# Performance work log

Measured on AMD Instinct MI355X. Metric: run time of the kernel, lower is better.

The kernel has to match this reference:

```python
import jax, jax.numpy as jnp
import numpy as np

T, B, I, H, R, O = 128, 32, 128, 128, 100, 64


def setup_inputs() -> dict:
    key = jax.random.key(0)
    ks = jax.random.split(key, 8)
    # xavier-ish / kaiming-ish scales so tanh doesn't saturate
    return {
        "x": jax.random.normal(ks[0], (T, B, I), jnp.float32),
        "C": jax.random.uniform(ks[1], (R, R), jnp.float32) / R,
        "W_ih": jax.random.normal(ks[2], (R, I, H), jnp.float32) * (1.0 / np.sqrt(I)),
        "W_hh": jax.random.normal(ks[3], (R, H, H), jnp.float32) * (1.0 / np.sqrt(H)),
        "W_rhh": jax.random.normal(ks[4], (R, H, H), jnp.float32) * (1.0 / np.sqrt(H)),
        "bias": jax.random.normal(ks[5], (R, H), jnp.float32) * 0.1,
        "W_out": jax.random.normal(ks[6], (R * H, O), jnp.float32) * (1.0 / np.sqrt(R * H)),
        "b_out": jax.random.normal(ks[7], (O,), jnp.float32) * 0.1,
    }


def reference(x, C, W_ih, W_hh, W_rhh, bias, b_out, W_out):
    seq_len, bs, _ = x.shape
    num_regions, hidden = bias.shape
    H0 = jnp.zeros((num_regions, bs, hidden), dtype=x.dtype)

    def step(Hprev, x_t):
        # input drive: per-region projection of the shared input
        inp = jnp.einsum('bi,rih->rbh', x_t, W_ih)
        # local recurrence
        loc = jnp.einsum('rbh,rhg->rbg', Hprev, W_hh)
        # connectome-weighted message sum: recurrent_sum[j] = sum_i C[i,j] * Hprev[i]
        msg = jnp.einsum('ij,ibh->jbh', C, Hprev)
        cross = jnp.einsum('rbh,rhg->rbg', msg, W_rhh)
        Ht = jnp.tanh(inp + loc + cross + bias[:, None, :])
        return Ht, Ht

    _, H_hist = jax.lax.scan(step, H0, x)          # [T, R, B, H]
    H_hist = H_hist.transpose(0, 2, 1, 3).reshape(seq_len, bs, num_regions * hidden)
    return H_hist @ W_out + b_out                   # [T, B, O]
```

## Files before the change

### kernel.cpp

```cpp
#include <hip/hip_runtime.h>
#include <hip/hip_bf16.h>

typedef unsigned char u8;
typedef unsigned short u16;
typedef __attribute__((ext_vector_type(8))) short bf16x8;
typedef __attribute__((ext_vector_type(8))) _Float16 f16x8;
typedef __attribute__((ext_vector_type(4))) float f32x4;
typedef __attribute__((ext_vector_type(2))) float f32x2;
typedef __attribute__((ext_vector_type(4))) int i32x4;
typedef __attribute__((ext_vector_type(2))) int i32x2;

#define T_ 128
#define B_ 32
#define I_ 128
#define H_ 128
#define R_ 100
#define O_ 64
#define NWG2 200
#define NRED 4
#define SLICE (R_*B_*H_)
#define ROWB  (B_*H_)
#define XOFF  (T_*B_*I_)
#define WOFF  (R_*H_*H_)
#define OOFF  (O_*R_*H_)
#define PB    (16*O_)

__device__ __forceinline__ float b2f(u16 u) {
  unsigned x = ((unsigned)u) << 16; float f; __builtin_memcpy(&f, &x, 4); return f;
}
__device__ __forceinline__ u16 f2b(float f) {
  unsigned x; __builtin_memcpy(&x, &f, 4);
  unsigned lsb = (x >> 16) & 1u;
  x += 0x7fffu + lsb;
  return (u16)(x >> 16);
}
__device__ __forceinline__ void split2(float f, u16& hi, u16& lo) {
  hi = f2b(f);
  lo = f2b(f - b2f(hi));
}
__device__ __forceinline__ u16 f2h(float f) {
  _Float16 h = (_Float16)f; u16 u; __builtin_memcpy(&u, &h, 2); return u;
}
__device__ __forceinline__ float h2f(u16 u) {
  _Float16 h; __builtin_memcpy(&h, &u, 2); return (float)h;
}
__device__ __forceinline__ void split2h(float f, u16& hi, u16& lo) {
  _Float16 h = (_Float16)f;
  _Float16 l = (_Float16)(f - (float)h);
  __builtin_memcpy(&hi, &h, 2); __builtin_memcpy(&lo, &l, 2);
}
__device__ __forceinline__ float fast_tanh(float v) {
  float a = fabsf(v);
  float e = __expf(-2.f * a);
  float th = (1.f - e) * __builtin_amdgcn_rcpf(1.f + e);
  return v < 0.f ? -th : th;
}

#if __has_builtin(__builtin_amdgcn_cvt_pk_f32_fp8) && __has_builtin(__builtin_amdgcn_cvt_pk_fp8_f32)
#define HW_FP8 1
#endif

__device__ __forceinline__ unsigned enc1_fp8(float f) {
  unsigned x; __builtin_memcpy(&x, &f, 4);
  unsigned s = (x >> 31) << 7;
  float a = fabsf(f);
  if (!(a < 464.f)) return s | 0x7E;
  if (a == 0.f) return s;
  int E = (int)((x >> 23) & 0xFF) - 127;
  if (E < -6) E = -6;
  float sc; unsigned sb = (unsigned)(127 + 3 - E) << 23; __builtin_memcpy(&sc, &sb, 4);
  int q = (int)rintf(a * sc);
  if (q == 16) { E += 1; q = 8; }
  if (E > 8) return s | 0x7E;
  unsigned ee, mm;
  if (q < 8) { ee = 0; mm = (unsigned)q; }
  else { ee = (unsigned)(E + 7); mm = (unsigned)(q - 8); }
  return s | (ee << 3) | mm;
}
__device__ __forceinline__ float dec1_fp8(unsigned b) {
  unsigned s = (b >> 7) & 1, ee = (b >> 3) & 0xF, mm = b & 7;
  float v;
  if (ee == 0) v = (float)mm * 0.001953125f;
  else { unsigned fb = ((ee + 120) << 23) | (mm << 20); __builtin_memcpy(&v, &fb, 4); }
  return s ? -v : v;
}
__device__ __forceinline__ void fp8x4_to_f32(unsigned u, float* o) {
#ifdef HW_FP8
  f32x2 a = __builtin_amdgcn_cvt_pk_f32_fp8((int)u, false);
  f32x2 b = __builtin_amdgcn_cvt_pk_f32_fp8((int)u, true);
  o[0] = a[0]; o[1] = a[1]; o[2] = b[0]; o[3] = b[1];
#else
  o[0] = dec1_fp8(u & 255); o[1] = dec1_fp8((u >> 8) & 255);
  o[2] = dec1_fp8((u >> 16) & 255); o[3] = dec1_fp8(u >> 24);
#endif
}
__device__ __forceinline__ unsigned f32x4_to_fp8(float f0, float f1, float f2, float f3) {
#ifdef HW_FP8
  int v = __builtin_amdgcn_cvt_pk_fp8_f32(f0, f1, 0, false);
  v = __builtin_amdgcn_cvt_pk_fp8_f32(f2, f3, v, true);
  return (unsigned)v;
#else
  return enc1_fp8(f0) | (enc1_fp8(f1) << 8) | (enc1_fp8(f2) << 16) | (enc1_fp8(f3) << 24);
#endif
}
__device__ __forceinline__ i32x4 pack16(const u16* p) {
  i32x4 o;
  #pragma unroll
  for (int g = 0; g < 4; ++g)
    o[g] = (int)f32x4_to_fp8(h2f(p[g*4+0]), h2f(p[g*4+1]), h2f(p[g*4+2]), h2f(p[g*4+3]));
  return o;
}

__device__ __forceinline__ void st16_sc(void* p, i32x4 v) {
  asm volatile("global_store_dwordx4 %0, %1, off sc1" :: "v"(p), "v"(v) : "memory");
}
__device__ __forceinline__ void ld4_issue(int& r, const void* p) {
  asm volatile("global_load_dword %0, %1, off sc1" : "=v"(r) : "v"(p));
}
__device__ __forceinline__ void wait_vm() { asm volatile("s_waitcnt vmcnt(0)" ::: "memory"); }
#define WAITV(N) do { asm volatile("s_waitcnt vmcnt(" #N ")" ::: "memory"); \
                      __builtin_amdgcn_sched_barrier(0); } while (0)

__device__ __forceinline__ float aldf(const float* p) {
  return __hip_atomic_load((float*)p, __ATOMIC_RELAXED, __HIP_MEMORY_SCOPE_AGENT);
}
__device__ __forceinline__ void astf(float* p, float v) {
  __hip_atomic_store(p, v, __ATOMIC_RELAXED, __HIP_MEMORY_SCOPE_AGENT);
}

__global__ void __launch_bounds__(256)
probe_dtype(const u16* __restrict__ x, int* __restrict__ mode)
{
  __shared__ int cnt;
  if (threadIdx.x == 0) cnt = 0;
  __syncthreads();
  int bad = 0;
  for (int i = threadIdx.x; i < 8192; i += 256) {
    int ex = (x[i] >> 7) & 0xFF;
    if (ex >= 134) ++bad;
  }
  atomicAdd(&cnt, bad);
  __syncthreads();
  if (threadIdx.x == 0) *mode = (cnt > 256) ? 1 : 0;
}

__device__ __forceinline__ float load_in(const void* p, size_t i, int f32) {
  return f32 ? ((const float*)p)[i] : b2f(((const u16*)p)[i]);
}

__global__ void __launch_bounds__(256)
conv_split(const void* __restrict__ src, u16* __restrict__ hi, u16* __restrict__ lo,
           const int* __restrict__ mode, int n)
{
  int i = blockIdx.x * 256 + threadIdx.x;
  if (i < n) { u16 h, l; split2(load_in(src, i, *mode), h, l); hi[i] = h; lo[i] = l; }
}

__global__ void __launch_bounds__(256)
conv_vec(const void* __restrict__ src, float* __restrict__ dst,
         const int* __restrict__ mode, int n)
{
  int i = blockIdx.x * 256 + threadIdx.x;
  if (i < n) dst[i] = load_in(src, i, *mode);
}

__global__ void __launch_bounds__(256)
transpose_kn2(const void* __restrict__ in, u16* __restrict__ ohi, u16* __restrict__ olo,
              int KK, int NN, const int* __restrict__ mode, int fmt)
{
  __shared__ float tile[32][33];
  const int f32 = *mode;
  int ntk = KK >> 5, ntn = NN >> 5;
  int bid = blockIdx.x;
  int m  = bid / (ntk * ntn);
  int rem = bid % (ntk * ntn);
  int kt = rem / ntn, nt = rem % ntn;
  size_t base = (size_t)m * KK * NN;
  int tid = threadIdx.x;
  int tc = tid & 31, tr0 = tid >> 5;
  #pragma unroll
  for (int rr = 0; rr < 4; ++rr) {
    int tr = tr0 + rr * 8;
    tile[tr][tc] = load_in(in, base + (size_t)(kt*32 + tr) * NN + nt*32 + tc, f32);
  }
  __syncthreads();
  #pragma unroll
  for (int rr = 0; rr < 4; ++rr) {
    int tr = tr0 + rr * 8;
    u16 h, l;
    if (fmt) split2h(tile[tc][tr], h, l); else split2(tile[tc][tr], h, l);
    size_t di = base + (size_t)(nt*32 + tr) * KK + kt*32 + tc;
    ohi[di] = h; olo[di] = l;
  }
}

__device__ __forceinline__ void wait_flags(const int* f, int cnt, int target, int tid) {
  if (tid < cnt) {
    int sp = 0;
    while (__hip_atomic_load((int*)&f[tid * 32], __ATOMIC_RELAXED, __HIP_MEMORY_SCOPE_AGENT) < target) {
      __builtin_amdgcn_s_sleep(2);
      if (++sp > (1 << 18)) break;
    }
  }
  asm volatile("" ::: "memory");
  __syncthreads();
}
__device__ __forceinline__ void poll1(const int* f, int target) {
  int sp = 0;
  while (__hip_atomic_load((int*)f, __ATOMIC_RELAXED, __HIP_MEMORY_SCOPE_AGENT) < target) {
    if (++sp > 48) __builtin_amdgcn_s_sleep(2);
    if (sp > (1 << 20)) break;
  }
  asm volatile("" ::: "memory");
}
__device__ __forceinline__ void post_flag(int* f, int v) {
  __hip_atomic_store(f, v, __ATOMIC_RELAXED, __HIP_MEMORY_SCOPE_AGENT);
}

__device__ __forceinline__ f32x4 mfma_(bf16x8 a, bf16x8 b, f32x4 c) {
  return __builtin_amdgcn_mfma_f32_16x16x32_bf16(a, b, c, 0, 0, 0);
}
__device__ __forceinline__ f32x4 mfma_h(f16x8 a, f16x8 b, f32x4 c) {
  return __builtin_amdgcn_mfma_f32_16x16x32_f16(a, b, c, 0, 0, 0);
}

#define MIXROW(Q, CI) do { \
  float c_ = csh[(CI)]; float tf_[4]; \
  fp8x4_to_f32((unsigned)(Q), tf_); \
  macc0 = fmaf(c_, tf_[0], macc0); macc1 = fmaf(c_, tf_[1], macc1); \
  macc2 = fmaf(c_, tf_[2], macc2); macc3 = fmaf(c_, tf_[3], macc3); \
} while (0)

#define ISSUE8(Q, P) do { _Pragma("unroll") \
  for (int k_ = 0; k_ < 8; ++k_) ld4_issue(Q[k_], (P) + (size_t)k_ * ROWB); } while (0)
#define ISSUE4(Q, P) do { _Pragma("unroll") \
  for (int k_ = 0; k_ < 4; ++k_) ld4_issue(Q[k_], (P) + (size_t)k_ * ROWB); } while (0)
#define PROC8(Q, CI) do { _Pragma("unroll") \
  for (int k_ = 0; k_ < 8; ++k_) MIXROW(Q[k_], (CI) + k_); } while (0)
#define PROC4(Q, CI) do { _Pragma("unroll") \
  for (int k_ = 0; k_ < 4; ++k_) MIXROW(Q[k_], (CI) + k_); } while (0)

__global__ void __launch_bounds__(512)
rnn_kernel(const u16* __restrict__ x,
           u8* __restrict__ Hb,
           const u16* __restrict__ WihT, const u16* __restrict__ WhhT,
           const u16* __restrict__ WrhhT,
           const float* __restrict__ Cf,
           const float* __restrict__ biasf,
           const u16* __restrict__ WoutT,
           float* __restrict__ part,
           u16* __restrict__ part2,
           const float* __restrict__ boutf,
           float* __restrict__ out, int* __restrict__ flags, int bigpart)
{
  const int w    = blockIdx.x;
  const int tid  = threadIdx.x;
  const int lane = tid & 63;
  const int wv   = tid >> 6;
  const int l15  = lane & 15;
  const int quad = lane >> 4;

  __shared__ __align__(16) u16 Hmhi[16 * 136];
  __shared__ __align__(16) u16 Hmlo[16 * 136];
  __shared__ __align__(16) u16 msgS[16 * 136];
  __shared__ __align__(16) u16 mS[16 * 128];
  __shared__ float csh[112];

  if (w >= NWG2) {
    const int aw = w - NWG2;
    for (int t = 0; t < T_; ++t) {
      wait_flags(flags + 1, NWG2, t + 1, tid);
      const float* pb = part + (size_t)(t & 1) * (NWG2 * PB);
      int e = aw * 512 + tid;
      int b = e >> 6, o = e & 63;
      int ue = b >> 4, bl = b & 15;
      float s = 0.f;
      #pragma unroll 4
      for (int r2 = 0; r2 < R_; ++r2)
        s += aldf(pb + (size_t)(r2 * 2 + ue) * PB + bl * O_ + o);
      out[(size_t)t * (B_*O_) + e] = s + boutf[o];
    }
    return;
  }

  const int r = w >> 1;
  const int u = w & 1;
  const int col = wv * 16 + l15;

  for (int e = tid; e < 16 * 136; e += 512) { Hmhi[e] = 0; Hmlo[e] = 0; }
  if (tid < R_) csh[tid] = Cf[(size_t)tid * R_ + r];
  __syncthreads();

  for (int t = 0; t < T_; ++t) {
    f32x4 accX = {0,0,0,0}, accH = {0,0,0,0};
    {
      const u16* Ax  = x + (size_t)t * (B_*I_) + (size_t)(u*16) * I_;
      const u16* Bw0 = WihT + (size_t)r * (H_*I_);
      const u16* Bw1 = WhhT + (size_t)r * (H_*H_);
      #pragma unroll
      for (int kk = 0; kk < 4; ++kk) {
        int koff = kk * 32 + quad * 8;
        {
          const u16* pa = Ax + (size_t)l15 * 128 + koff;
          bf16x8 ah = *(const bf16x8*)pa, al = *(const bf16x8*)(pa + XOFF);
          const u16* pb = Bw0 + (size_t)col * 128 + koff;
          bf16x8 bh = *(const bf16x8*)pb, bl = *(const bf16x8*)(pb + WOFF);
          accX = mfma_(al,bh, mfma_(ah,bl, mfma_(ah,bh, accX)));
        }
        {
          bf16x8 ah = *(const bf16x8*)(&Hmhi[l15 * 136 + koff]);
          bf16x8 al = *(const bf16x8*)(&Hmlo[l15 * 136 + koff]);
          const u16* pb = Bw1 + (size_t)col * 128 + koff;
          bf16x8 bh = *(const bf16x8*)pb, bl = *(const bf16x8*)(pb + WOFF);
          accH = mfma_(al,bh, mfma_(ah,bl, mfma_(ah,bh, accH)));
        }
      }
    }

    if (t > 0) {
      if (tid < R_) poll1(&flags[(tid * 2 + u) * 32], t);
      __syncthreads();

      const u8* Hs = Hb + (size_t)((t + 1) & 1) * SLICE
                   + (size_t)(u*16 + (tid >> 5)) * H_ + (tid & 31) * 4;
      float macc0=0.f, macc1=0.f, macc2=0.f, macc3=0.f;
      int bufA[8], bufB[8], bufC[8];
      const u8* pI = Hs;
      ISSUE8(bufA, pI); pI += (size_t)8 * ROWB;
      ISSUE8(bufB, pI); pI += (size_t)8 * ROWB;
      ISSUE8(bufC, pI); pI += (size_t)8 * ROWB;
      int ci = 0;
      for (int it = 0; it < 3; ++it) {
        WAITV(16); PROC8(bufA, ci); ci += 8; ISSUE8(bufA, pI); pI += (size_t)8 * ROWB;
        WAITV(16); PROC8(bufB, ci); ci += 8; ISSUE8(bufB, pI); pI += (size_t)8 * ROWB;
        WAITV(16); PROC8(bufC, ci); ci += 8; ISSUE8(bufC, pI); pI += (size_t)8 * ROWB;
      }
      WAITV(16); PROC8(bufA, 72); ISSUE4(bufA, pI);
      WAITV(12); PROC8(bufB, 80);
      WAITV(4);  PROC8(bufC, 88);
      WAITV(0);  PROC4(bufA, 96);

      union { u16 h[4]; unsigned long long v; } mw;
      mw.h[0]=f2h(macc0); mw.h[1]=f2h(macc1); mw.h[2]=f2h(macc2); mw.h[3]=f2h(macc3);
      *(unsigned long long*)&msgS[(tid >> 5) * 136 + (tid & 31) * 4] = mw.v;
      __syncthreads();

      {
        const u16* Bw2 = WrhhT + (size_t)r * (H_*H_);
        #pragma unroll
        for (int kk = 0; kk < 4; ++kk) {
          int koff = kk * 32 + quad * 8;
          f16x8 a0 = *(const f16x8*)(&msgS[l15 * 136 + koff]);
          const u16* pb = Bw2 + (size_t)col * 128 + koff;
          f16x8 bh = *(const f16x8*)pb, bl = *(const f16x8*)(pb + WOFF);
          accX = mfma_h(a0, bl, mfma_h(a0, bh, accX));
        }
      }
    } else {
      __syncthreads();
    }

    {
      float bs = biasf[r*H_ + col];
      #pragma unroll
      for (int rr = 0; rr < 4; ++rr) {
        int br = quad*4 + rr;
        u16 h, l;
        float v = fast_tanh(accX[rr] + accH[rr] + bs);
        split2(v, h, l);
        Hmhi[br*136 + col] = h; Hmlo[br*136 + col] = l;
        mS[br*128 + col] = f2h(v);
      }
    }
    __syncthreads();

    if (tid < 64) {
      int row = tid >> 2, c = (tid & 3) * 32;
      u8* Hn = Hb + (size_t)(t & 1) * SLICE + (size_t)r * ROWB
             + (size_t)(u*16 + row) * H_ + c;
      const u16* p = &mS[row * 128 + c];
      st16_sc(Hn,      pack16(p));
      st16_sc(Hn + 16, pack16(p + 16));
      wait_vm();
      if (tid == 0) post_flag(&flags[w * 32 + 0], t + 1);
    }

    {
      if (wv >= 4) {
        const int o = (wv - 4) * 16 + l15;
        const u16* Bo = WoutT + (size_t)o * (R_*H_) + (size_t)r * H_;
        f32x4 y0 = {0,0,0,0};
        #pragma unroll
        for (int kk = 0; kk < 4; ++kk) {
          int koff = kk * 32 + quad * 8;
          bf16x8 ah = *(const bf16x8*)(&Hmhi[l15 * 136 + koff]);
          bf16x8 al = *(const bf16x8*)(&Hmlo[l15 * 136 + koff]);
          bf16x8 bh = *(const bf16x8*)(Bo + koff);
          bf16x8 bl = *(const bf16x8*)(Bo + OOFF + koff);
          y0 = mfma_(al,bh, mfma_(ah,bl, mfma_(ah,bh, y0)));
        }
        if (bigpart) {
          u16* pp = part2 + ((size_t)t * R_ + r) * (B_*O_);
          #pragma unroll
          for (int rr = 0; rr < 4; ++rr)
            pp[(u*16 + quad*4 + rr)*O_ + o] = f2b(y0[rr]);
        } else {
          float* pp = part + (size_t)(t & 1) * (NWG2 * PB) + (size_t)w * PB;
          #pragma unroll
          for (int rr = 0; rr < 4; ++rr)
            astf(pp + (quad*4 + rr)*O_ + o, y0[rr]);
        }
      }
      if (!bigpart) {
        __syncthreads();
        if (tid == 0) post_flag(&flags[w * 32 + 1], t + 1);
      }
    }
  }
}

__global__ void __launch_bounds__(256)
reduce_out(const u16* __restrict__ part2, const float* __restrict__ boutf,
           float* __restrict__ out)
{
  const int t = blockIdx.x, tid = threadIdx.x;
  const u16* base = part2 + (size_t)t * R_ * (B_*O_) + tid * 8;
  float acc[8] = {0,0,0,0,0,0,0,0};
  for (int r2 = 0; r2 < R_; ++r2) {
    bf16x8 v = *(const bf16x8*)(base + (size_t)r2 * (B_*O_));
    #pragma unroll
    for (int j = 0; j < 8; ++j) acc[j] += b2f((u16)v[j]);
  }
  int e = tid * 8;
  #pragma unroll
  for (int j = 0; j < 8; ++j)
    out[(size_t)t * (B_*O_) + e + j] = acc[j] + boutf[(e + j) & (O_-1)];
}

extern "C" void kernel_launch(void* const* d_in, const int* in_sizes, int n_in,
                              void* d_out, int out_size, void* d_ws, size_t ws_size,
                              hipStream_t stream) {
  const void* xp    = d_in[0];
  const void* Cp    = d_in[1];
  const void* Wih   = d_in[2];
  const void* Whh   = d_in[3];
  const void* Wrhh  = d_in[4];
  const void* biasp = d_in[5];
  const void* Wout  = d_in[6];
  const void* boutp = d_in[7];
  float* outp = (float*)d_out;

  char* ws = (char*)d_ws;
  size_t off = 0;
  auto carve = [&](size_t bytes) -> void* {
    void* p = ws + off;
    off += (bytes + 255) & ~(size_t)255;
    return p;
  };
  u16*   xb    = (u16*)carve((size_t)2 * XOFF * 2);
  u8*    Hb    = (u8*)carve((size_t)2 * SLICE);
  u16*   wihT  = (u16*)carve((size_t)2 * WOFF * 2);
  u16*   whhT  = (u16*)carve((size_t)2 * WOFF * 2);
  u16*   wrhhT = (u16*)carve((size_t)2 * WOFF * 2);
  u16*   woutT = (u16*)carve((size_t)2 * OOFF * 2);
  float* cfp   = (float*)carve((size_t)R_ * R_ * 4);
  float* biasf = (float*)carve((size_t)R_ * H_ * 4);
  float* boutf = (float*)carve((size_t)O_ * 4);
  float* partp = (float*)carve((size_t)2 * NWG2 * PB * 4);
  int*   flagp = (int*)carve((size_t)256 * 32 * 4);
  int*   modep = (int*)carve(256);
  size_t part2_bytes = (size_t)T_ * R_ * B_ * O_ * 2;
  u16*   part2 = (u16*)(ws + off);
  int bigpart = (off + part2_bytes) <= ws_size;

  hipMemsetAsync(flagp, 0, (size_t)256 * 32 * 4, stream);

  probe_dtype<<<dim3(1), dim3(256), 0, stream>>>((const u16*)xp, modep);
  conv_split<<<dim3((XOFF + 255)/256), dim3(256), 0, stream>>>(xp, xb, xb + XOFF, modep, XOFF);
  conv_vec<<<dim3((R_*H_ + 255)/256), dim3(256), 0, stream>>>(biasp, biasf, modep, R_*H_);
  conv_vec<<<dim3(1), dim3(256), 0, stream>>>(boutp, boutf, modep, O_);
  conv_vec<<<dim3((R_*R_ + 255)/256), dim3(256), 0, stream>>>(Cp, cfp, modep, R_*R_);

  transpose_kn2<<<dim3(R_ * 16), dim3(256), 0, stream>>>(Wih,  wihT,  wihT  + WOFF, I_, H_, modep, 0);
  transpose_kn2<<<dim3(R_ * 16), dim3(256), 0, stream>>>(Whh,  whhT,  whhT  + WOFF, H_, H_, modep, 0);
  transpose_kn2<<<dim3(R_ * 16), dim3(256), 0, stream>>>(Wrhh, wrhhT, wrhhT + WOFF, H_, H_, modep, 1);
  transpose_kn2<<<dim3(800),     dim3(256), 0, stream>>>(Wout, woutT, woutT + OOFF, R_ * H_, O_, modep, 0);

  int nblk = bigpart ? NWG2 : (NWG2 + NRED);
  rnn_kernel<<<dim3(nblk), dim3(512), 0, stream>>>(
      xb, Hb, wihT, whhT, wrhhT, cfp, biasf, woutT,
      partp, part2, boutf, outp, flagp, bigpart);

  if (bigpart)
    reduce_out<<<dim3(T_), dim3(256), 0, stream>>>(part2, boutf, outp);
}
```

Measured before the change: 1.218 ms.

## Stage per-step hidden state into per-XCD copies for local L2 reads

At each step, up to four workgroups on each XCD copy the previous hidden state from the shared buffer, which is read with sc1 loads, into a per-XCD staged buffer, then post per-chunk flags. All workgroups on that XCD then read the connectome mix inputs from the staged copy using sc0 loads, which should hit that XCD's L2 instead of going coherent across dies. The W_rhh tiles are also loaded before the mix wait so they overlap the polling. The cost is an extra copy and flag handshake on the critical path of every timestep, plus reliance on the hardware XCC id register and on co-residency assumptions.

```diff
diff --git a/kernel.cpp b/kernel.cpp
--- a/kernel.cpp
+++ b/kernel.cpp
@@ -24,6 +24,11 @@
 #define WOFF  (R_*H_*H_)
 #define OOFF  (O_*R_*H_)
 #define PB    (16*O_)
+#define UHALF 2048
+#define SBUF  (R_*UHALF)
+#define CHUNK (50*UHALF)
+#define SFBASE 6400
+#define XCNTOFF 7168
 
 __device__ __forceinline__ float b2f(u16 u) {
   unsigned x = ((unsigned)u) << 16; float f; __builtin_memcpy(&f, &x, 4); return f;
@@ -114,8 +119,11 @@
 __device__ __forceinline__ void st16_sc(void* p, i32x4 v) {
   asm volatile("global_store_dwordx4 %0, %1, off sc1" :: "v"(p), "v"(v) : "memory");
 }
-__device__ __forceinline__ void ld4_issue(int& r, const void* p) {
-  asm volatile("global_load_dword %0, %1, off sc1" : "=v"(r) : "v"(p));
+__device__ __forceinline__ void ld4_issue0(int& r, const void* p) {
+  asm volatile("global_load_dword %0, %1, off sc0" : "=v"(r) : "v"(p));
+}
+__device__ __forceinline__ void ld16_issue1(i32x4& r, const void* p) {
+  asm volatile("global_load_dwordx4 %0, %1, off sc1" : "=v"(r) : "v"(p));
 }
 __device__ __forceinline__ void wait_vm() { asm volatile("s_waitcnt vmcnt(0)" ::: "memory"); }
 #define WAITV(N) do { asm volatile("s_waitcnt vmcnt(" #N ")" ::: "memory"); \
@@ -232,9 +240,9 @@
 } while (0)
 
 #define ISSUE8(Q, P) do { _Pragma("unroll") \
-  for (int k_ = 0; k_ < 8; ++k_) ld4_issue(Q[k_], (P) + (size_t)k_ * ROWB); } while (0)
+  for (int k_ = 0; k_ < 8; ++k_) ld4_issue0(Q[k_], (P) + (size_t)k_ * UHALF); } while (0)
 #define ISSUE4(Q, P) do { _Pragma("unroll") \
-  for (int k_ = 0; k_ < 4; ++k_) ld4_issue(Q[k_], (P) + (size_t)k_ * ROWB); } while (0)
+  for (int k_ = 0; k_ < 4; ++k_) ld4_issue0(Q[k_], (P) + (size_t)k_ * UHALF); } while (0)
 #define PROC8(Q, CI) do { _Pragma("unroll") \
   for (int k_ = 0; k_ < 8; ++k_) MIXROW(Q[k_], (CI) + k_); } while (0)
 #define PROC4(Q, CI) do { _Pragma("unroll") \
@@ -243,6 +251,7 @@
 __global__ void __launch_bounds__(512)
 rnn_kernel(const u16* __restrict__ x,
            u8* __restrict__ Hb,
+           u8* __restrict__ staged,
            const u16* __restrict__ WihT, const u16* __restrict__ WhhT,
            const u16* __restrict__ WrhhT,
            const float* __restrict__ Cf,
@@ -265,6 +274,7 @@
   __shared__ __align__(16) u16 msgS[16 * 136];
   __shared__ __align__(16) u16 mS[16 * 128];
   __shared__ float csh[112];
+  __shared__ int shRank, shN;
 
   if (w >= NWG2) {
     const int aw = w - NWG2;
@@ -283,6 +293,13 @@
     return;
   }
 
+  int xcd;
+  asm volatile("s_getreg_b32 %0, hwreg(HW_REG_XCC_ID)" : "=s"(xcd));
+  xcd &= 7;
+  if (tid == 0)
+    shRank = __hip_atomic_fetch_add(&flags[XCNTOFF + xcd], 1,
+                                    __ATOMIC_RELAXED, __HIP_MEMORY_SCOPE_AGENT);
+
   const int r = w >> 1;
   const int u = w & 1;
   const int col = wv * 16 + l15;
@@ -290,6 +307,7 @@
   for (int e = tid; e < 16 * 136; e += 512) { Hmhi[e] = 0; Hmlo[e] = 0; }
   if (tid < R_) csh[tid] = Cf[(size_t)tid * R_ + r];
   __syncthreads();
+  const int rank = shRank;
 
   for (int t = 0; t < T_; ++t) {
     f32x4 accX = {0,0,0,0}, accH = {0,0,0,0};
@@ -318,22 +336,74 @@
     }
 
     if (t > 0) {
-      if (tid < R_) poll1(&flags[(tid * 2 + u) * 32], t);
+      if (t == 1) {
+        if (tid == 0) {
+          int c = __hip_atomic_load(&flags[XCNTOFF + xcd],
+                                    __ATOMIC_RELAXED, __HIP_MEMORY_SCOPE_AGENT);
+          shN = c < 1 ? 1 : (c > 4 ? 4 : c);
+        }
+        __syncthreads();
+      }
+      const int par = (t + 1) & 1;
+
+      f16x8 w2h[4], w2l[4];
+      {
+        const u16* Bw2 = WrhhT + (size_t)r * (H_*H_);
+        #pragma unroll
+        for (int kk = 0; kk < 4; ++kk) {
+          const u16* pb = Bw2 + (size_t)col * 128 + kk*32 + quad*8;
+          w2h[kk] = *(const f16x8*)pb;
+          w2l[kk] = *(const f16x8*)(pb + WOFF);
+        }
+      }
+
+      if (rank < 4) {
+        const int N = shN;
+        for (int cc = rank; cc < 4; cc += N) {
+          const int su = cc & 1, sc2 = cc >> 1;
+          if (tid < 50) poll1(&flags[(((sc2*50 + tid) << 1) | su) * 32], t);
+          __syncthreads();
+          const u8* srcb = Hb + (size_t)par * SLICE;
+          u8* dstb = staged + ((((size_t)xcd << 1) | par) * 2 + su) * SBUF
+                   + (size_t)sc2 * CHUNK;
+          i32x4 qq[13];
+          #pragma unroll
+          for (int k = 0; k < 13; ++k) {
+            int le = tid * 16 + k * 8192;
+            int le2 = le < CHUNK ? le : 0;
+            int reg = sc2 * 50 + (le2 >> 11);
+            ld16_issue1(qq[k], srcb + (size_t)reg * ROWB + su * UHALF + (le2 & 2047));
+          }
+          WAITV(0);
+          #pragma unroll
+          for (int k = 0; k < 13; ++k) {
+            int le = tid * 16 + k * 8192;
+            if (le < CHUNK) *(i32x4*)(dstb + le) = qq[k];
+          }
+          wait_vm();
+          __syncthreads();
+          if (tid == 0)
+            post_flag(&flags[SFBASE + ((xcd * 2 + par) << 2) + cc], t);
+        }
+      }
+
+      if (tid < 2)
+        poll1(&flags[SFBASE + ((xcd * 2 + par) << 2) + u + (tid << 1)], t);
       __syncthreads();
 
-      const u8* Hs = Hb + (size_t)((t + 1) & 1) * SLICE
-                   + (size_t)(u*16 + (tid >> 5)) * H_ + (tid & 31) * 4;
+      const u8* Ms = staged + ((((size_t)xcd << 1) | par) * 2 + u) * SBUF
+                   + (size_t)(tid >> 5) * 128 + (tid & 31) * 4;
       float macc0=0.f, macc1=0.f, macc2=0.f, macc3=0.f;
       int bufA[8], bufB[8], bufC[8];
-      const u8* pI = Hs;
-      ISSUE8(bufA, pI); pI += (size_t)8 * ROWB;
-      ISSUE8(bufB, pI); pI += (size_t)8 * ROWB;
-      ISSUE8(bufC, pI); pI += (size_t)8 * ROWB;
+      const u8* pI = Ms;
+      ISSUE8(bufA, pI); pI += (size_t)8 * UHALF;
+      ISSUE8(bufB, pI); pI += (size_t)8 * UHALF;
+      ISSUE8(bufC, pI); pI += (size_t)8 * UHALF;
       int ci = 0;
       for (int it = 0; it < 3; ++it) {
-        WAITV(16); PROC8(bufA, ci); ci += 8; ISSUE8(bufA, pI); pI += (size_t)8 * ROWB;
-        WAITV(16); PROC8(bufB, ci); ci += 8; ISSUE8(bufB, pI); pI += (size_t)8 * ROWB;
-        WAITV(16); PROC8(bufC, ci); ci += 8; ISSUE8(bufC, pI); pI += (size_t)8 * ROWB;
+        WAITV(16); PROC8(bufA, ci); ci += 8; ISSUE8(bufA, pI); pI += (size_t)8 * UHALF;
+        WAITV(16); PROC8(bufB, ci); ci += 8; ISSUE8(bufB, pI); pI += (size_t)8 * UHALF;
+        WAITV(16); PROC8(bufC, ci); ci += 8; ISSUE8(bufC, pI); pI += (size_t)8 * UHALF;
       }
       WAITV(16); PROC8(bufA, 72); ISSUE4(bufA, pI);
       WAITV(12); PROC8(bufB, 80);
@@ -345,16 +415,11 @@
       *(unsigned long long*)&msgS[(tid >> 5) * 136 + (tid & 31) * 4] = mw.v;
       __syncthreads();
 
-      {
-        const u16* Bw2 = WrhhT + (size_t)r * (H_*H_);
-        #pragma unroll
-        for (int kk = 0; kk < 4; ++kk) {
-          int koff = kk * 32 + quad * 8;
-          f16x8 a0 = *(const f16x8*)(&msgS[l15 * 136 + koff]);
-          const u16* pb = Bw2 + (size_t)col * 128 + koff;
-          f16x8 bh = *(const f16x8*)pb, bl = *(const f16x8*)(pb + WOFF);
-          accX = mfma_h(a0, bl, mfma_h(a0, bh, accX));
-        }
+      #pragma unroll
+      for (int kk = 0; kk < 4; ++kk) {
+        int koff = kk * 32 + quad * 8;
+        f16x8 a0 = *(const f16x8*)(&msgS[l15 * 136 + koff]);
+        accX = mfma_h(a0, w2l[kk], mfma_h(a0, w2h[kk], accX));
       }
     } else {
       __syncthreads();
@@ -459,6 +524,7 @@
   };
   u16*   xb    = (u16*)carve((size_t)2 * XOFF * 2);
   u8*    Hb    = (u8*)carve((size_t)2 * SLICE);
+  u8*    stg   = (u8*)carve((size_t)8 * 2 * 2 * SBUF);
   u16*   wihT  = (u16*)carve((size_t)2 * WOFF * 2);
   u16*   whhT  = (u16*)carve((size_t)2 * WOFF * 2);
   u16*   wrhhT = (u16*)carve((size_t)2 * WOFF * 2);
@@ -488,7 +554,7 @@
 
   int nblk = bigpart ? NWG2 : (NWG2 + NRED);
   rnn_kernel<<<dim3(nblk), dim3(512), 0, stream>>>(
-      xb, Hb, wihT, whhT, wrhhT, cfp, biasf, woutT,
+      xb, Hb, stg, wihT, whhT, wrhhT, cfp, biasf, woutT,
       partp, part2, boutf, outp, flagp, bigpart);
 
   if (bigpart)
```

New measurement: 1.602 ms. +31.5%, slower.

## Hoist weights into registers and use per-XCD leader barrier with non-coherent loads

Applied to the files above, without the earlier changes.

Loads all per-region weight fragments (W_ih, W_hh, W_rhh, W_out) into registers once before the time loop instead of re-reading them from global memory every step. Replaces the per-workgroup poll of 100 producer flags with a hierarchical barrier: one leader workgroup per XCD polls all 200 producers, does an acquire fence, then posts a per-XCD flag that the other workgroups on that XCD wait on. The hidden-state gather loads change from the sc1 cache hint to sc0. Launch bounds now request 2 blocks per SM, which limits register use. The risks are register spills from the large weight arrays, and coherence problems if the XCD-local L2 does not see the peer stores.

```diff
diff --git a/kernel.cpp b/kernel.cpp
--- a/kernel.cpp
+++ b/kernel.cpp
@@ -8,7 +8,6 @@
 typedef __attribute__((ext_vector_type(4))) float f32x4;
 typedef __attribute__((ext_vector_type(2))) float f32x2;
 typedef __attribute__((ext_vector_type(4))) int i32x4;
-typedef __attribute__((ext_vector_type(2))) int i32x2;
 
 #define T_ 128
 #define B_ 32
@@ -24,6 +23,8 @@
 #define WOFF  (R_*H_*H_)
 #define OOFF  (O_*R_*H_)
 #define PB    (16*O_)
+#define SFBASE 6400
+#define XCNTOFF 7168
 
 __device__ __forceinline__ float b2f(u16 u) {
   unsigned x = ((unsigned)u) << 16; float f; __builtin_memcpy(&f, &x, 4); return f;
@@ -114,8 +115,8 @@
 __device__ __forceinline__ void st16_sc(void* p, i32x4 v) {
   asm volatile("global_store_dwordx4 %0, %1, off sc1" :: "v"(p), "v"(v) : "memory");
 }
-__device__ __forceinline__ void ld4_issue(int& r, const void* p) {
-  asm volatile("global_load_dword %0, %1, off sc1" : "=v"(r) : "v"(p));
+__device__ __forceinline__ void ld4_issue0(int& r, const void* p) {
+  asm volatile("global_load_dword %0, %1, off sc0" : "=v"(r) : "v"(p));
 }
 __device__ __forceinline__ void wait_vm() { asm volatile("s_waitcnt vmcnt(0)" ::: "memory"); }
 #define WAITV(N) do { asm volatile("s_waitcnt vmcnt(" #N ")" ::: "memory"); \
@@ -232,15 +233,15 @@
 } while (0)
 
 #define ISSUE8(Q, P) do { _Pragma("unroll") \
-  for (int k_ = 0; k_ < 8; ++k_) ld4_issue(Q[k_], (P) + (size_t)k_ * ROWB); } while (0)
+  for (int k_ = 0; k_ < 8; ++k_) ld4_issue0(Q[k_], (P) + (size_t)k_ * ROWB); } while (0)
 #define ISSUE4(Q, P) do { _Pragma("unroll") \
-  for (int k_ = 0; k_ < 4; ++k_) ld4_issue(Q[k_], (P) + (size_t)k_ * ROWB); } while (0)
+  for (int k_ = 0; k_ < 4; ++k_) ld4_issue0(Q[k_], (P) + (size_t)k_ * ROWB); } while (0)
 #define PROC8(Q, CI) do { _Pragma("unroll") \
   for (int k_ = 0; k_ < 8; ++k_) MIXROW(Q[k_], (CI) + k_); } while (0)
 #define PROC4(Q, CI) do { _Pragma("unroll") \
   for (int k_ = 0; k_ < 4; ++k_) MIXROW(Q[k_], (CI) + k_); } while (0)
 
-__global__ void __launch_bounds__(512)
+__global__ void __launch_bounds__(512, 2)
 rnn_kernel(const u16* __restrict__ x,
            u8* __restrict__ Hb,
            const u16* __restrict__ WihT, const u16* __restrict__ WhhT,
@@ -265,6 +266,7 @@
   __shared__ __align__(16) u16 msgS[16 * 136];
   __shared__ __align__(16) u16 mS[16 * 128];
   __shared__ float csh[112];
+  __shared__ int shRank;
 
   if (w >= NWG2) {
     const int aw = w - NWG2;
@@ -283,6 +285,13 @@
     return;
   }
 
+  int xcd;
+  asm volatile("s_getreg_b32 %0, hwreg(HW_REG_XCC_ID)" : "=s"(xcd));
+  xcd &= 7;
+  if (tid == 0)
+    shRank = __hip_atomic_fetch_add(&flags[XCNTOFF + xcd], 1,
+                                    __ATOMIC_RELAXED, __HIP_MEMORY_SCOPE_AGENT);
+
   const int r = w >> 1;
   const int u = w & 1;
   const int col = wv * 16 + l15;
@@ -290,38 +299,67 @@
   for (int e = tid; e < 16 * 136; e += 512) { Hmhi[e] = 0; Hmlo[e] = 0; }
   if (tid < R_) csh[tid] = Cf[(size_t)tid * R_ + r];
   __syncthreads();
+  const int rank = shRank;
+
+  bf16x8 w0h[4], w0l[4], w1h[4], w1l[4];
+  f16x8  w2h[4], w2l[4];
+  bf16x8 boh[4], bol[4];
+  {
+    const u16* B0 = WihT  + (size_t)r * (H_*I_) + (size_t)col * 128;
+    const u16* B1 = WhhT  + (size_t)r * (H_*H_) + (size_t)col * 128;
+    const u16* B2 = WrhhT + (size_t)r * (H_*H_) + (size_t)col * 128;
+    const int o = (wv >= 4) ? ((wv - 4) * 16 + l15) : l15;
+    const u16* Bo = WoutT + (size_t)o * (R_*H_) + (size_t)r * H_;
+    #pragma unroll
+    for (int kk = 0; kk < 4; ++kk) {
+      int koff = kk * 32 + quad * 8;
+      w0h[kk] = *(const bf16x8*)(B0 + koff);
+      w0l[kk] = *(const bf16x8*)(B0 + WOFF + koff);
+      w1h[kk] = *(const bf16x8*)(B1 + koff);
+      w1l[kk] = *(const bf16x8*)(B1 + WOFF + koff);
+      w2h[kk] = *(const f16x8*)(B2 + koff);
+      w2l[kk] = *(const f16x8*)(B2 + WOFF + koff);
+      boh[kk] = *(const bf16x8*)(Bo + koff);
+      bol[kk] = *(const bf16x8*)(Bo + OOFF + koff);
+    }
+  }
+  const float bs = biasf[r*H_ + col];
 
   for (int t = 0; t < T_; ++t) {
     f32x4 accX = {0,0,0,0}, accH = {0,0,0,0};
     {
-      const u16* Ax  = x + (size_t)t * (B_*I_) + (size_t)(u*16) * I_;
-      const u16* Bw0 = WihT + (size_t)r * (H_*I_);
-      const u16* Bw1 = WhhT + (size_t)r * (H_*H_);
+      const u16* Ax = x + (size_t)t * (B_*I_) + (size_t)(u*16) * I_;
       #pragma unroll
       for (int kk = 0; kk < 4; ++kk) {
         int koff = kk * 32 + quad * 8;
-        {
-          const u16* pa = Ax + (size_t)l15 * 128 + koff;
-          bf16x8 ah = *(const bf16x8*)pa, al = *(const bf16x8*)(pa + XOFF);
-          const u16* pb = Bw0 + (size_t)col * 128 + koff;
-          bf16x8 bh = *(const bf16x8*)pb, bl = *(const bf16x8*)(pb + WOFF);
-          accX = mfma_(al,bh, mfma_(ah,bl, mfma_(ah,bh, accX)));
+        const u16* pa = Ax + (size_t)l15 * 128 + koff;
+        bf16x8 ah = *(const bf16x8*)pa, al = *(const bf16x8*)(pa + XOFF);
+        accX = mfma_(al, w0h[kk], mfma_(ah, w0l[kk], mfma_(ah, w0h[kk], accX)));
+        bf16x8 hh = *(const bf16x8*)(&Hmhi[l15 * 136 + koff]);
+        bf16x8 hl = *(const bf16x8*)(&Hmlo[l15 * 136 + koff]);
+        accH = mfma_(hl, w1h[kk], mfma_(hh, w1l[kk], mfma_(hh, w1h[kk], accH)));
+      }
+    }
+
+    if (t > 0) {
+      const int par = (t + 1) & 1;
+      int* invf = &flags[SFBASE + ((xcd << 1) + par) * 32];
+
+      if (rank == 0) {
+        if (tid < NWG2) poll1(&flags[tid * 32], t);
+        __syncthreads();
+        if (tid == 0) {
+          __builtin_amdgcn_fence(__ATOMIC_ACQUIRE, "agent");
+          wait_vm();
+          post_flag(invf, t);
         }
-        {
-          bf16x8 ah = *(const bf16x8*)(&Hmhi[l15 * 136 + koff]);
-          bf16x8 al = *(const bf16x8*)(&Hmlo[l15 * 136 + koff]);
-          const u16* pb = Bw1 + (size_t)col * 128 + koff;
-          bf16x8 bh = *(const bf16x8*)pb, bl = *(const bf16x8*)(pb + WOFF);
-          accH = mfma_(al,bh, mfma_(ah,bl, mfma_(ah,bh, accH)));
-        }
-      }
-    }
-
-    if (t > 0) {
-      if (tid < R_) poll1(&flags[(tid * 2 + u) * 32], t);
-      __syncthreads();
-
-      const u8* Hs = Hb + (size_t)((t + 1) & 1) * SLICE
+        __syncthreads();
+      } else {
+        if (tid == 0) poll1(invf, t);
+        __syncthreads();
+      }
+
+      const u8* Hs = Hb + (size_t)par * SLICE
                    + (size_t)(u*16 + (tid >> 5)) * H_ + (tid & 31) * 4;
       float macc0=0.f, macc1=0.f, macc2=0.f, macc3=0.f;
       int bufA[8], bufB[8], bufC[8];
@@ -345,23 +383,17 @@
       *(unsigned long long*)&msgS[(tid >> 5) * 136 + (tid & 31) * 4] = mw.v;
       __syncthreads();
 
-      {
-        const u16* Bw2 = WrhhT + (size_t)r * (H_*H_);
-        #pragma unroll
-        for (int kk = 0; kk < 4; ++kk) {
-          int koff = kk * 32 + quad * 8;
-          f16x8 a0 = *(const f16x8*)(&msgS[l15 * 136 + koff]);
-          const u16* pb = Bw2 + (size_t)col * 128 + koff;
-          f16x8 bh = *(const f16x8*)pb, bl = *(const f16x8*)(pb + WOFF);
-          accX = mfma_h(a0, bl, mfma_h(a0, bh, accX));
-        }
+      #pragma unroll
+      for (int kk = 0; kk < 4; ++kk) {
+        int koff = kk * 32 + quad * 8;
+        f16x8 a0 = *(const f16x8*)(&msgS[l15 * 136 + koff]);
+        accX = mfma_h(a0, w2l[kk], mfma_h(a0, w2h[kk], accX));
       }
     } else {
       __syncthreads();
     }
 
     {
-      float bs = biasf[r*H_ + col];
       #pragma unroll
       for (int rr = 0; rr < 4; ++rr) {
         int br = quad*4 + rr;
@@ -388,16 +420,13 @@
     {
       if (wv >= 4) {
         const int o = (wv - 4) * 16 + l15;
-        const u16* Bo = WoutT + (size_t)o * (R_*H_) + (size_t)r * H_;
         f32x4 y0 = {0,0,0,0};
         #pragma unroll
         for (int kk = 0; kk < 4; ++kk) {
           int koff = kk * 32 + quad * 8;
           bf16x8 ah = *(const bf16x8*)(&Hmhi[l15 * 136 + koff]);
           bf16x8 al = *(const bf16x8*)(&Hmlo[l15 * 136 + koff]);
-          bf16x8 bh = *(const bf16x8*)(Bo + koff);
-          bf16x8 bl = *(const bf16x8*)(Bo + OOFF + koff);
-          y0 = mfma_(al,bh, mfma_(ah,bl, mfma_(ah,bh, y0)));
+          y0 = mfma_(al, boh[kk], mfma_(ah, bol[kk], mfma_(ah, boh[kk], y0)));
         }
         if (bigpart) {
           u16* pp = part2 + ((size_t)t * R_ + r) * (B_*O_);
```

Result: faster. 1.010 ms (-17.0%).
